# Kernel tuning notes

Hardware: AMD Instinct MI355X
Metric: run time of the kernel (lower is better)

The kernel has to match this reference:

```python
import jax, jax.numpy as jnp
import numpy as np

N_NODES = 50000
N_EDGES = 800000
D_NODE = 64
D_ATTR = 16
D_T = 16
D_OUT = 128


def setup_inputs() -> dict:
    key = jax.random.key(0)
    ks = jax.random.split(key, 8)
    x = jax.random.normal(ks[0], (N_NODES, D_NODE), dtype=jnp.float32)
    edge_index = jax.random.randint(ks[1], (2, N_EDGES), 0, N_NODES, dtype=jnp.int64)
    edge_attr = jax.random.normal(ks[2], (N_EDGES, D_ATTR), dtype=jnp.float32)
    edge_t = jax.random.normal(ks[3], (N_EDGES, D_T), dtype=jnp.float32)
    d_msg = D_NODE + D_ATTR + D_T  # 96, = in_channels[0]
    Wm = jax.random.normal(ks[4], (d_msg, D_OUT), dtype=jnp.float32) / np.sqrt(d_msg)
    bm = jnp.zeros((D_OUT,), dtype=jnp.float32)
    Wr = jax.random.normal(ks[5], (D_NODE, D_OUT), dtype=jnp.float32) / np.sqrt(D_NODE)
    br = jnp.zeros((D_OUT,), dtype=jnp.float32)
    return {"x": x, "edge_index": edge_index, "edge_attr": edge_attr,
            "edge_t": edge_t, "Wm": Wm, "bm": bm, "Wr": Wr, "br": br}


def reference(x, edge_index, edge_attr, edge_t, Wm, bm, Wr, br):
    row, col = edge_index[0], edge_index[1]
    # gather source node feats and concat edge features -> [E, 96]
    msg = jnp.concatenate([x[col], edge_attr, edge_t], axis=1)
    # scatter-sum messages to destination nodes -> [N, 96]
    agg = jax.ops.segment_sum(msg, row, num_segments=x.shape[0])
    x_j = agg @ Wm + bm          # lin_m
    x_i = x @ Wr + br            # lin_r
    out = 0.5 * x_j + x_i        # normalize=False path
    return out
```

## Files before the change

kernel.cpp:

```cpp
#include <hip/hip_runtime.h>
#include <hip/hip_bf16.h>

#define NN 50000
#define NE 800000
#define D_NODE 64
#define D_MSG 96
#define D_K 160
#define D_OUT 128
#define KP 168

#define SCAN_BLOCKS 49

typedef __attribute__((ext_vector_type(8))) short bf16x8;
typedef __attribute__((ext_vector_type(4))) float f32x4;

#define CNT_OFF  0
#define OFF_OFF  200000
#define CUR_OFF  400000
#define PERM_OFF 600000
#define A_OFF    7000064
#define BSUM_OFF 23000064
#define WS_NEEDED (BSUM_OFF + SCAN_BLOCKS * 4)

__device__ __forceinline__ unsigned short f2bf(float f) {
    __hip_bfloat16 h = __float2bfloat16(f);
    union { __hip_bfloat16 h; unsigned short u; } c; c.h = h;
    return c.u;
}
__device__ __forceinline__ float bf2f(unsigned int u) {
    union { unsigned int i; float f; } c; c.i = u << 16; return c.f;
}

__global__ __launch_bounds__(256) void xcast_kernel(
    const float* __restrict__ x, unsigned short* __restrict__ A)
{
    int t = blockIdx.x * 256 + threadIdx.x;
    if (t >= NN * 16) return;
    int node = t >> 4, c4 = t & 15;
    float4 v = *(const float4*)(x + (size_t)node * D_NODE + c4 * 4);
    uint2 pk;
    pk.x = (unsigned)f2bf(v.x) | ((unsigned)f2bf(v.y) << 16);
    pk.y = (unsigned)f2bf(v.z) | ((unsigned)f2bf(v.w) << 16);
    *(uint2*)(A + (size_t)node * D_K + D_MSG + c4 * 4) = pk;
}

__global__ __launch_bounds__(256) void hist_kernel(
    const int* __restrict__ row, int* __restrict__ cnt)
{
    int e = blockIdx.x * blockDim.x + threadIdx.x;
    if (e < NE) atomicAdd(&cnt[row[e]], 1);
}

__global__ __launch_bounds__(256) void scanA_kernel(
    const int* __restrict__ cnt, int* __restrict__ bsum)
{
    const int t = threadIdx.x, b = blockIdx.x;
    const int idx4 = b * 256 + t;
    int s = 0;
    if (idx4 < NN / 4) {
        int4 c = ((const int4*)cnt)[idx4];
        s = c.x + c.y + c.z + c.w;
    }
    for (int d = 32; d > 0; d >>= 1) s += __shfl_down(s, d);
    __shared__ int wsum[4];
    if ((t & 63) == 0) wsum[t >> 6] = s;
    __syncthreads();
    if (t == 0) bsum[b] = wsum[0] + wsum[1] + wsum[2] + wsum[3];
}

__global__ __launch_bounds__(64) void scanB_kernel(int* __restrict__ bsum)
{
    const int t = threadIdx.x;
    int v = (t < SCAN_BLOCKS) ? bsum[t] : 0;
    int orig = v;
    for (int d = 1; d < 64; d <<= 1) {
        int u = __shfl_up(v, d);
        if (t >= d) v += u;
    }
    if (t < SCAN_BLOCKS) bsum[t] = v - orig;
}

__global__ __launch_bounds__(256) void scanC_kernel(
    const int* __restrict__ cnt, const int* __restrict__ bsum,
    int* __restrict__ off, int* __restrict__ cur)
{
    const int t = threadIdx.x, b = blockIdx.x;
    const int idx4 = b * 256 + t;
    const bool valid = (idx4 < NN / 4);
    int4 c = make_int4(0, 0, 0, 0);
    if (valid) c = ((const int4*)cnt)[idx4];
    int s = c.x + c.y + c.z + c.w;

    const int lane = t & 63, w = t >> 6;
    int v = s;
    for (int d = 1; d < 64; d <<= 1) {
        int u = __shfl_up(v, d);
        if (lane >= d) v += u;
    }
    __shared__ int wsum[4];
    if (lane == 63) wsum[w] = v;
    __syncthreads();
    int woff = 0;
    for (int i = 0; i < 4; ++i) if (i < w) woff += wsum[i];

    if (valid) {
        int excl = (v - s) + woff + bsum[b];
        int4 o;
        o.x = excl;
        o.y = o.x + c.x;
        o.z = o.y + c.y;
        o.w = o.z + c.z;
        ((int4*)off)[idx4] = o;
        ((int4*)cur)[idx4] = o;
    }
}

__global__ __launch_bounds__(256) void bucket_kernel(
    const int* __restrict__ row, const int* __restrict__ col,
    int* __restrict__ cur, int2* __restrict__ perm)
{
    int e = blockIdx.x * blockDim.x + threadIdx.x;
    if (e >= NE) return;
    int pos = atomicAdd(&cur[row[e]], 1);
    perm[pos] = make_int2(e, col[e]);
}

__global__ __launch_bounds__(256) void gather_kernel(
    const float* __restrict__ ea,
    const float* __restrict__ et,
    const int*  __restrict__ off,
    const int*  __restrict__ cnt,
    const int2* __restrict__ perm,
    unsigned short* __restrict__ A)
{
    const int node = blockIdx.x * 4 + (threadIdx.x >> 6);
    const int lane = threadIdx.x & 63;
    if (node >= NN) return;

    const int beg = off[node];
    const int end = beg + cnt[node];

    const int half = lane >> 5;
    const int hl   = lane & 31;
    const float* ebase = ((lane >> 4) & 1) ? et : ea;
    const int ecol = lane & 15;

    float accx0 = 0.f, accx1 = 0.f;
    float acce  = 0.f;

    int j = beg;
    if ((j & 1) && j < end) {
        int2 p = perm[j];
        if (half == 0) {
            unsigned xv = *(const unsigned*)(A + (size_t)p.y * D_K + D_MSG + hl * 2);
            accx0 += bf2f(xv & 0xffffu);
            accx1 += bf2f(xv >> 16);
            acce  += ebase[(size_t)p.x * 16 + ecol];
        }
        ++j;
    }
    for (; j + 4 <= end; j += 4) {
        int4 q0 = *(const int4*)(perm + j);
        int4 q1 = *(const int4*)(perm + j + 2);
        int c01 = half ? q0.w : q0.y;
        int e01 = half ? q0.z : q0.x;
        int c23 = half ? q1.w : q1.y;
        int e23 = half ? q1.z : q1.x;
        unsigned xv0 = *(const unsigned*)(A + (size_t)c01 * D_K + D_MSG + hl * 2);
        unsigned xv1 = *(const unsigned*)(A + (size_t)c23 * D_K + D_MSG + hl * 2);
        float ev0 = ebase[(size_t)e01 * 16 + ecol];
        float ev1 = ebase[(size_t)e23 * 16 + ecol];
        accx0 += bf2f(xv0 & 0xffffu) + bf2f(xv1 & 0xffffu);
        accx1 += bf2f(xv0 >> 16)     + bf2f(xv1 >> 16);
        acce  += ev0 + ev1;
    }
    if (j + 2 <= end) {
        int4 q0 = *(const int4*)(perm + j);
        int c01 = half ? q0.w : q0.y;
        int e01 = half ? q0.z : q0.x;
        unsigned xv0 = *(const unsigned*)(A + (size_t)c01 * D_K + D_MSG + hl * 2);
        accx0 += bf2f(xv0 & 0xffffu);
        accx1 += bf2f(xv0 >> 16);
        acce  += ebase[(size_t)e01 * 16 + ecol];
        j += 2;
    }
    if (j < end) {
        int2 p = perm[j];
        if (half == 0) {
            unsigned xv = *(const unsigned*)(A + (size_t)p.y * D_K + D_MSG + hl * 2);
            accx0 += bf2f(xv & 0xffffu);
            accx1 += bf2f(xv >> 16);
            acce  += ebase[(size_t)p.x * 16 + ecol];
        }
    }

    accx0 += __shfl_xor(accx0, 32);
    accx1 += __shfl_xor(accx1, 32);
    acce  += __shfl_xor(acce, 32);

    unsigned short* dst = A + (size_t)node * D_K;
    if (half == 0) {
        unsigned pk = (unsigned)f2bf(0.5f * accx0)
                    | ((unsigned)f2bf(0.5f * accx1) << 16);
        *(unsigned*)(dst + hl * 2) = pk;
    } else {
        dst[D_NODE + hl] = f2bf(0.5f * acce);
    }
}

__global__ __launch_bounds__(256) void mfma_dense_kernel(
    const unsigned short* __restrict__ A,
    const float* __restrict__ Wm,
    const float* __restrict__ bm,
    const float* __restrict__ Wr,
    const float* __restrict__ br,
    float*       __restrict__ out)
{
    __shared__ unsigned short Bt[D_OUT * KP];

    for (int i = threadIdx.x; i < D_K * D_OUT; i += 256) {
        int k = i >> 7, n = i & 127;
        float v = (k < D_MSG) ? Wm[i] : Wr[i - D_MSG * D_OUT];
        Bt[n * KP + k] = f2bf(v);
    }
    __syncthreads();

    const int l   = threadIdx.x & 63;
    const int wid = threadIdx.x >> 6;
    const int wm  = wid & 1;
    const int wn  = wid >> 1;
    const int lr  = l & 15;
    const int lk  = (l >> 4) << 3;

    bf16x8 bq[4][5];
#pragma unroll
    for (int nf = 0; nf < 4; ++nf) {
        int c = wn * 64 + nf * 16 + lr;
#pragma unroll
        for (int ks = 0; ks < 5; ++ks)
            bq[nf][ks] = *(const bf16x8*)(&Bt[c * KP + ks * 32 + lk]);
    }

    const int row0 = blockIdx.x * 64 + wm * 32;

    f32x4 acc[2][4];
#pragma unroll
    for (int mf = 0; mf < 2; ++mf)
#pragma unroll
        for (int nf = 0; nf < 4; ++nf)
            acc[mf][nf] = (f32x4){0.f, 0.f, 0.f, 0.f};

#pragma unroll
    for (int ks = 0; ks < 5; ++ks) {
#pragma unroll
        for (int mf = 0; mf < 2; ++mf) {
            int row = row0 + mf * 16 + lr;
            if (row > NN - 1) row = NN - 1;
            bf16x8 af = *(const bf16x8*)(A + (size_t)row * D_K + ks * 32 + lk);
#pragma unroll
            for (int nf = 0; nf < 4; ++nf)
                acc[mf][nf] = __builtin_amdgcn_mfma_f32_16x16x32_bf16(
                    af, bq[nf][ks], acc[mf][nf], 0, 0, 0);
        }
    }

#pragma unroll
    for (int nf = 0; nf < 4; ++nf) {
        int c = wn * 64 + nf * 16 + lr;
        float bias = 0.5f * bm[c] + br[c];
#pragma unroll
        for (int mf = 0; mf < 2; ++mf) {
            int rbase = row0 + mf * 16 + ((l >> 4) << 2);
#pragma unroll
            for (int r = 0; r < 4; ++r) {
                int row = rbase + r;
                if (row < NN) out[(size_t)row * D_OUT + c] = acc[mf][nf][r] + bias;
            }
        }
    }
}

extern "C" void kernel_launch(void* const* d_in, const int* in_sizes, int n_in,
                              void* d_out, int out_size, void* d_ws, size_t ws_size,
                              hipStream_t stream) {
    const float* x  = (const float*)d_in[0];
    const int*   ei = (const int*)d_in[1];
    const float* ea = (const float*)d_in[2];
    const float* et = (const float*)d_in[3];
    const float* Wm = (const float*)d_in[4];
    const float* bm = (const float*)d_in[5];
    const float* Wr = (const float*)d_in[6];
    const float* br = (const float*)d_in[7];
    float* out = (float*)d_out;
    const int* row = ei;
    const int* col = ei + NE;

    char* ws = (char*)d_ws;
    int*  cnt  = (int*)(ws + CNT_OFF);
    int*  off  = (int*)(ws + OFF_OFF);
    int*  cur  = (int*)(ws + CUR_OFF);
    int2* perm = (int2*)(ws + PERM_OFF);
    int*  bsum = (int*)(ws + BSUM_OFF);
    unsigned short* A = (unsigned short*)(ws + A_OFF);

    hipMemsetAsync(cnt, 0, NN * sizeof(int), stream);
    xcast_kernel <<<(NN * 16 + 255) / 256, 256, 0, stream>>>(x, A);
    hist_kernel  <<<(NE + 255) / 256, 256, 0, stream>>>(row, cnt);
    scanA_kernel <<<SCAN_BLOCKS, 256, 0, stream>>>(cnt, bsum);
    scanB_kernel <<<1, 64, 0, stream>>>(bsum);
    scanC_kernel <<<SCAN_BLOCKS, 256, 0, stream>>>(cnt, bsum, off, cur);
    bucket_kernel<<<(NE + 255) / 256, 256, 0, stream>>>(row, col, cur, perm);
    gather_kernel<<<(NN + 3) / 4, 256, 0, stream>>>(ea, et, off, cnt, perm, A);
    mfma_dense_kernel<<<(NN + 63) / 64, 256, 0, stream>>>(A, Wm, bm, Wr, br, out);
}
```

Before: 179.0 us.

## Fuse cast with histogram and scan passes, unroll gather with dual accumulators

Merges the x-to-bf16 cast and the row histogram into one launch, and folds the block-sum scan into scanC so each block scans the block sums itself. This removes two kernel launches and their serialization gaps. The gather loop now processes 8 edges per iteration into two accumulator sets, for more memory-level parallelism. The A matrix is re-laid out with a 192-element stride and the x part first, and the small bsum buffer is placed inside a not-yet-written slice of A. That placement relies on the scans finishing before the gather writes that slice, and the wider stride increases the bytes the dense kernel touches.

```diff
diff --git a/kernel.cpp b/kernel.cpp
--- a/kernel.cpp
+++ b/kernel.cpp
@@ -6,10 +6,12 @@
 #define D_NODE 64
 #define D_MSG 96
 #define D_K 160
+#define AS 192
 #define D_OUT 128
 #define KP 168
 
 #define SCAN_BLOCKS 49
+#define XCAST_BLOCKS 3125
 
 typedef __attribute__((ext_vector_type(8))) short bf16x8;
 typedef __attribute__((ext_vector_type(4))) float f32x4;
@@ -19,8 +21,7 @@
 #define CUR_OFF  400000
 #define PERM_OFF 600000
 #define A_OFF    7000064
-#define BSUM_OFF 23000064
-#define WS_NEEDED (BSUM_OFF + SCAN_BLOCKS * 4)
+#define BSUM_OFF (A_OFF + 128)
 
 __device__ __forceinline__ unsigned short f2bf(float f) {
     __hip_bfloat16 h = __float2bfloat16(f);
@@ -31,24 +32,23 @@
     union { unsigned int i; float f; } c; c.i = u << 16; return c.f;
 }
 
-__global__ __launch_bounds__(256) void xcast_kernel(
-    const float* __restrict__ x, unsigned short* __restrict__ A)
-{
-    int t = blockIdx.x * 256 + threadIdx.x;
-    if (t >= NN * 16) return;
-    int node = t >> 4, c4 = t & 15;
-    float4 v = *(const float4*)(x + (size_t)node * D_NODE + c4 * 4);
-    uint2 pk;
-    pk.x = (unsigned)f2bf(v.x) | ((unsigned)f2bf(v.y) << 16);
-    pk.y = (unsigned)f2bf(v.z) | ((unsigned)f2bf(v.w) << 16);
-    *(uint2*)(A + (size_t)node * D_K + D_MSG + c4 * 4) = pk;
-}
-
-__global__ __launch_bounds__(256) void hist_kernel(
+__global__ __launch_bounds__(256) void prep_kernel(
+    const float* __restrict__ x, unsigned short* __restrict__ A,
     const int* __restrict__ row, int* __restrict__ cnt)
 {
-    int e = blockIdx.x * blockDim.x + threadIdx.x;
-    if (e < NE) atomicAdd(&cnt[row[e]], 1);
+    const int b = blockIdx.x;
+    if (b < XCAST_BLOCKS) {
+        int t = b * 256 + threadIdx.x;
+        int node = t >> 4, c4 = t & 15;
+        float4 v = *(const float4*)(x + (size_t)node * D_NODE + c4 * 4);
+        uint2 pk;
+        pk.x = (unsigned)f2bf(v.x) | ((unsigned)f2bf(v.y) << 16);
+        pk.y = (unsigned)f2bf(v.z) | ((unsigned)f2bf(v.w) << 16);
+        *(uint2*)(A + (size_t)node * AS + c4 * 4) = pk;
+    } else {
+        int e = (b - XCAST_BLOCKS) * 256 + threadIdx.x;
+        if (e < NE) atomicAdd(&cnt[row[e]], 1);
+    }
 }
 
 __global__ __launch_bounds__(256) void scanA_kernel(
@@ -68,23 +68,26 @@
     if (t == 0) bsum[b] = wsum[0] + wsum[1] + wsum[2] + wsum[3];
 }
 
-__global__ __launch_bounds__(64) void scanB_kernel(int* __restrict__ bsum)
-{
-    const int t = threadIdx.x;
-    int v = (t < SCAN_BLOCKS) ? bsum[t] : 0;
-    int orig = v;
-    for (int d = 1; d < 64; d <<= 1) {
-        int u = __shfl_up(v, d);
-        if (t >= d) v += u;
-    }
-    if (t < SCAN_BLOCKS) bsum[t] = v - orig;
-}
-
 __global__ __launch_bounds__(256) void scanC_kernel(
     const int* __restrict__ cnt, const int* __restrict__ bsum,
     int* __restrict__ off, int* __restrict__ cur)
 {
+    __shared__ int s_boff;
+    __shared__ int wsum[4];
     const int t = threadIdx.x, b = blockIdx.x;
+
+    if (t < 64) {
+        int v = (t < SCAN_BLOCKS) ? bsum[t] : 0;
+        int orig = v;
+        for (int d = 1; d < 64; d <<= 1) {
+            int u = __shfl_up(v, d);
+            if (t >= d) v += u;
+        }
+        int excl = v - orig;
+        int want = __shfl(excl, b);
+        if (t == 0) s_boff = want;
+    }
+
     const int idx4 = b * 256 + t;
     const bool valid = (idx4 < NN / 4);
     int4 c = make_int4(0, 0, 0, 0);
@@ -97,14 +100,13 @@
         int u = __shfl_up(v, d);
         if (lane >= d) v += u;
     }
-    __shared__ int wsum[4];
     if (lane == 63) wsum[w] = v;
     __syncthreads();
     int woff = 0;
     for (int i = 0; i < 4; ++i) if (i < w) woff += wsum[i];
 
     if (valid) {
-        int excl = (v - s) + woff + bsum[b];
+        int excl = (v - s) + woff + s_boff;
         int4 o;
         o.x = excl;
         o.y = o.x + c.x;
@@ -145,66 +147,76 @@
     const float* ebase = ((lane >> 4) & 1) ? et : ea;
     const int ecol = lane & 15;
 
-    float accx0 = 0.f, accx1 = 0.f;
-    float acce  = 0.f;
+    float accx0 = 0.f, accx1 = 0.f, acce = 0.f;
+    float accx0b = 0.f, accx1b = 0.f, acceb = 0.f;
+
+#define EDGE_PAIR(q, ax0, ax1, ae)                                          \
+    {                                                                       \
+        int cc = half ? (q).w : (q).y;                                      \
+        int ee = half ? (q).z : (q).x;                                      \
+        unsigned xv = *(const unsigned*)(A + (size_t)cc * AS + hl * 2);     \
+        float ev = ebase[(size_t)ee * 16 + ecol];                           \
+        ax0 += bf2f(xv & 0xffffu);                                          \
+        ax1 += bf2f(xv >> 16);                                              \
+        ae  += ev;                                                          \
+    }
 
     int j = beg;
     if ((j & 1) && j < end) {
         int2 p = perm[j];
         if (half == 0) {
-            unsigned xv = *(const unsigned*)(A + (size_t)p.y * D_K + D_MSG + hl * 2);
+            unsigned xv = *(const unsigned*)(A + (size_t)p.y * AS + hl * 2);
             accx0 += bf2f(xv & 0xffffu);
             accx1 += bf2f(xv >> 16);
             acce  += ebase[(size_t)p.x * 16 + ecol];
         }
         ++j;
     }
-    for (; j + 4 <= end; j += 4) {
+    for (; j + 8 <= end; j += 8) {
         int4 q0 = *(const int4*)(perm + j);
         int4 q1 = *(const int4*)(perm + j + 2);
-        int c01 = half ? q0.w : q0.y;
-        int e01 = half ? q0.z : q0.x;
-        int c23 = half ? q1.w : q1.y;
-        int e23 = half ? q1.z : q1.x;
-        unsigned xv0 = *(const unsigned*)(A + (size_t)c01 * D_K + D_MSG + hl * 2);
-        unsigned xv1 = *(const unsigned*)(A + (size_t)c23 * D_K + D_MSG + hl * 2);
-        float ev0 = ebase[(size_t)e01 * 16 + ecol];
-        float ev1 = ebase[(size_t)e23 * 16 + ecol];
-        accx0 += bf2f(xv0 & 0xffffu) + bf2f(xv1 & 0xffffu);
-        accx1 += bf2f(xv0 >> 16)     + bf2f(xv1 >> 16);
-        acce  += ev0 + ev1;
+        int4 q2 = *(const int4*)(perm + j + 4);
+        int4 q3 = *(const int4*)(perm + j + 6);
+        EDGE_PAIR(q0, accx0, accx1, acce)
+        EDGE_PAIR(q1, accx0b, accx1b, acceb)
+        EDGE_PAIR(q2, accx0, accx1, acce)
+        EDGE_PAIR(q3, accx0b, accx1b, acceb)
+    }
+    if (j + 4 <= end) {
+        int4 q0 = *(const int4*)(perm + j);
+        int4 q1 = *(const int4*)(perm + j + 2);
+        EDGE_PAIR(q0, accx0, accx1, acce)
+        EDGE_PAIR(q1, accx0b, accx1b, acceb)
+        j += 4;
     }
     if (j + 2 <= end) {
         int4 q0 = *(const int4*)(perm + j);
-        int c01 = half ? q0.w : q0.y;
-        int e01 = half ? q0.z : q0.x;
-        unsigned xv0 = *(const unsigned*)(A + (size_t)c01 * D_K + D_MSG + hl * 2);
-        accx0 += bf2f(xv0 & 0xffffu);
-        accx1 += bf2f(xv0 >> 16);
-        acce  += ebase[(size_t)e01 * 16 + ecol];
+        EDGE_PAIR(q0, accx0, accx1, acce)
         j += 2;
     }
     if (j < end) {
         int2 p = perm[j];
         if (half == 0) {
-            unsigned xv = *(const unsigned*)(A + (size_t)p.y * D_K + D_MSG + hl * 2);
+            unsigned xv = *(const unsigned*)(A + (size_t)p.y * AS + hl * 2);
             accx0 += bf2f(xv & 0xffffu);
             accx1 += bf2f(xv >> 16);
             acce  += ebase[(size_t)p.x * 16 + ecol];
         }
     }
-
+#undef EDGE_PAIR
+
+    accx0 += accx0b; accx1 += accx1b; acce += acceb;
     accx0 += __shfl_xor(accx0, 32);
     accx1 += __shfl_xor(accx1, 32);
     acce  += __shfl_xor(acce, 32);
 
-    unsigned short* dst = A + (size_t)node * D_K;
+    unsigned short* dst = A + (size_t)node * AS;
     if (half == 0) {
         unsigned pk = (unsigned)f2bf(0.5f * accx0)
                     | ((unsigned)f2bf(0.5f * accx1) << 16);
-        *(unsigned*)(dst + hl * 2) = pk;
+        *(unsigned*)(dst + D_NODE + hl * 2) = pk;
     } else {
-        dst[D_NODE + hl] = f2bf(0.5f * acce);
+        dst[2 * D_NODE + hl] = f2bf(0.5f * acce);
     }
 }
 
@@ -220,7 +232,7 @@
 
     for (int i = threadIdx.x; i < D_K * D_OUT; i += 256) {
         int k = i >> 7, n = i & 127;
-        float v = (k < D_MSG) ? Wm[i] : Wr[i - D_MSG * D_OUT];
+        float v = (k < D_NODE) ? Wr[i] : Wm[i - D_NODE * D_OUT];
         Bt[n * KP + k] = f2bf(v);
     }
     __syncthreads();
@@ -256,7 +268,7 @@
         for (int mf = 0; mf < 2; ++mf) {
             int row = row0 + mf * 16 + lr;
             if (row > NN - 1) row = NN - 1;
-            bf16x8 af = *(const bf16x8*)(A + (size_t)row * D_K + ks * 32 + lk);
+            bf16x8 af = *(const bf16x8*)(A + (size_t)row * AS + ks * 32 + lk);
 #pragma unroll
             for (int nf = 0; nf < 4; ++nf)
                 acc[mf][nf] = __builtin_amdgcn_mfma_f32_16x16x32_bf16(
@@ -304,10 +316,8 @@
     unsigned short* A = (unsigned short*)(ws + A_OFF);
 
     hipMemsetAsync(cnt, 0, NN * sizeof(int), stream);
-    xcast_kernel <<<(NN * 16 + 255) / 256, 256, 0, stream>>>(x, A);
-    hist_kernel  <<<(NE + 255) / 256, 256, 0, stream>>>(row, cnt);
+    prep_kernel  <<<2 * XCAST_BLOCKS, 256, 0, stream>>>(x, A, row, cnt);
     scanA_kernel <<<SCAN_BLOCKS, 256, 0, stream>>>(cnt, bsum);
-    scanB_kernel <<<1, 64, 0, stream>>>(bsum);
     scanC_kernel <<<SCAN_BLOCKS, 256, 0, stream>>>(cnt, bsum, off, cur);
     bucket_kernel<<<(NE + 255) / 256, 256, 0, stream>>>(row, col, cur, perm);
     gather_kernel<<<(NN + 3) / 4, 256, 0, stream>>>(ea, et, off, cnt, perm, A);
```

Result: faster. 167.2 us (-6.6%).
